# Kernel optimization log

Hardware: AMD Instinct MI355X
Metric: run time of the kernel (lower is better)

Reference implementation:

```python
import jax, jax.numpy as jnp
import numpy as np

BETA_THRESH = 0.1   # threshold fraction in forward
BETA_IPOT = 0.5     # IPOT entropic beta
ITERATION = 30


def setup_inputs() -> dict:
    key = jax.random.key(0)
    k1, k2 = jax.random.split(key)
    bs, n, m, d = 64, 512, 512, 768
    return {
        "local_features_1": jax.random.normal(k1, (bs, n, d), dtype=jnp.float32),
        "local_features_2": jax.random.normal(k2, (bs, m, d), dtype=jnp.float32),
    }


def _wasserstein_loss(x, y):
    # x: (bs, n, d), y: (bs, m, d)
    # cost_matrix_batch_torch normalizes over the feature dim (dim=1 of bs*d*n layout)
    xn = x / (jnp.linalg.norm(x, axis=2, keepdims=True) + 1e-12)
    yn = y / (jnp.linalg.norm(y, axis=2, keepdims=True) + 1e-12)
    # cost_matrix returns (1 - cos).transpose(2,1); forward transposes back -> (bs, n, m)
    cos_distance = 1.0 - jnp.einsum("bnd,bmd->bnm", xn, yn)
    # global min/max threshold + relu
    min_score = cos_distance.min()
    max_score = cos_distance.max()
    threshold = min_score + BETA_THRESH * (max_score - min_score)
    C = jax.nn.relu(cos_distance - threshold)  # (bs, n, m)
    bs, n, m = C.shape
    A = jnp.exp(-C / BETA_IPOT)
    T0 = jnp.ones((bs, n, m), dtype=C.dtype)
    sigma0 = jnp.full((bs, m, 1), 1.0 / m, dtype=C.dtype)

    def step(carry, _):
        T, sigma = carry
        Q = A * T                                      # (bs, n, m)
        delta = 1.0 / (n * jnp.matmul(Q, sigma))       # (bs, n, 1)
        a = jnp.matmul(jnp.swapaxes(Q, 1, 2), delta)   # (bs, m, 1)
        sigma = 1.0 / (m * a)                          # (bs, m, 1)
        T = delta * Q * jnp.swapaxes(sigma, 1, 2)      # (bs, n, m)
        return (T, sigma), None

    (T, _), _ = jax.lax.scan(step, (T0, sigma0), None, length=ITERATION)
    # batch_trace(C^T @ T) == sum_ij C_ij * T_ij per batch element
    distance = jnp.einsum("bnm,bnm->b", C, T)
    # IPOT_distance returns -distance; loss is its mean
    return (-distance).mean()


def reference(local_features_1, local_features_2):
    return _wasserstein_loss(local_features_1, local_features_2)
```

## Files before the change

kernel.cpp:

```cpp
#include <hip/hip_runtime.h>
#include <hip/hip_fp16.h>

#define NN 512
#define DD 768

typedef _Float16 half8 __attribute__((ext_vector_type(8)));
typedef _Float16 half4 __attribute__((ext_vector_type(4)));
typedef _Float16 half2v __attribute__((ext_vector_type(2)));
typedef float f32x4 __attribute__((ext_vector_type(4)));

__device__ __forceinline__ int f2ord(float f) {
  int i = __float_as_int(f);
  return i < 0 ? (i ^ 0x7fffffff) : i;
}
__device__ __forceinline__ float ord2f(int i) {
  return __int_as_float(i < 0 ? (i ^ 0x7fffffff) : i);
}

__device__ __forceinline__ void glds16(const void* g, void* l) {
  __builtin_amdgcn_global_load_lds((const __attribute__((address_space(1))) void*)g,
                                   (__attribute__((address_space(3))) void*)l, 16, 0, 0);
}

__global__ __launch_bounds__(256) void k_norm(const float* __restrict__ f1,
                                              const float* __restrict__ f2,
                                              __half* __restrict__ xn,
                                              __half* __restrict__ yn,
                                              int* __restrict__ meta,
                                              int* __restrict__ cnt) {
  if (blockIdx.x == 0) {
    int t = threadIdx.x;
    if (t == 0) { meta[0] = 0x7fffffff; meta[1] = 0x80000000; cnt[1024] = 0; }
    if (t < 64) cnt[t * 16] = 0;
  }
  int row = blockIdx.x * 4 + (threadIdx.x >> 6);
  int lane = threadIdx.x & 63;
  int r = row & 32767;
  const float* src = (row < 32768 ? f1 : f2) + (size_t)r * DD;
  __half* dst = (row < 32768 ? xn : yn) + (size_t)r * DD;
  f32x4 v0 = *(const f32x4*)(src + lane * 4);
  f32x4 v1 = *(const f32x4*)(src + lane * 4 + 256);
  f32x4 v2 = *(const f32x4*)(src + lane * 4 + 512);
  float s = v0[0]*v0[0] + v0[1]*v0[1] + v0[2]*v0[2] + v0[3]*v0[3]
          + v1[0]*v1[0] + v1[1]*v1[1] + v1[2]*v1[2] + v1[3]*v1[3]
          + v2[0]*v2[0] + v2[1]*v2[1] + v2[2]*v2[2] + v2[3]*v2[3];
  #pragma unroll
  for (int m = 1; m < 64; m <<= 1) s += __shfl_xor(s, m, 64);
  float f = 1.0f / (sqrtf(s) + 1e-12f);
  union U { __half2 h2[2]; uint2 u; };
  U u0, u1, u2;
  u0.h2[0] = __floats2half2_rn(v0[0]*f, v0[1]*f); u0.h2[1] = __floats2half2_rn(v0[2]*f, v0[3]*f);
  u1.h2[0] = __floats2half2_rn(v1[0]*f, v1[1]*f); u1.h2[1] = __floats2half2_rn(v1[2]*f, v1[3]*f);
  u2.h2[0] = __floats2half2_rn(v2[0]*f, v2[1]*f); u2.h2[1] = __floats2half2_rn(v2[2]*f, v2[3]*f);
  *(uint2*)(dst + lane * 4)       = u0.u;
  *(uint2*)(dst + lane * 4 + 256) = u1.u;
  *(uint2*)(dst + lane * 4 + 512) = u2.u;
}

#define FOR16(X) X(0) X(1) X(2) X(3) X(4) X(5) X(6) X(7) X(8) X(9) X(10) X(11) X(12) X(13) X(14) X(15)

#define AGLD(p) __hip_atomic_load((p), __ATOMIC_RELAXED, __HIP_MEMORY_SCOPE_AGENT)
#define AGST(p, v) __hip_atomic_store((p), (v), __ATOMIC_RELAXED, __HIP_MEMORY_SCOPE_AGENT)

struct IpotLds {
  float xs[128];
  float ys[NN];
  _Float16 zs[NN];
  _Float16 csh[8][520];
  float wred[8];
};
union MainLds {
  _Float16 Bs[2][16384];
  _Float16 At[4][8192];
  float mm[16];
  int mmi[16];
  IpotLds ip;
};

__global__ __launch_bounds__(512, 2) void k_main(const __half* __restrict__ xn,
                                                 const __half* __restrict__ yn,
                                                 int* __restrict__ meta,
                                                 int* __restrict__ cnt,
                                                 int* __restrict__ gmm,
                                                 unsigned* __restrict__ gpart,
                                                 float* __restrict__ gdist) {
  __shared__ __align__(16) MainLds u;
  const int blk = blockIdx.x;
  const int b = blk & 63, qq = blk >> 6;
  const int tid = threadIdx.x;
  const int sv = tid >> 6, lane = tid & 63;
  const int fr = lane & 15;
  const int g8 = (lane >> 4) * 8;
  const int r0 = sv * 16;
  const int c0 = lane * 8;
  const __half* xnb = xn + ((size_t)b * NN + qq * 128 + sv * 16) * DD;
  const __half* ynb = yn + (size_t)b * NN * DD;

  f32x4 acc[32] = {};
#define STAGE(bf, kk) { \
    const __half* ys_ = ynb + (size_t)(sv * 64 + lane) * DD + (kk); \
    glds16(ys_ +  0, (char*)u.Bs[bf] +         sv * 1024); \
    glds16(ys_ +  8, (char*)u.Bs[bf] +  8192 + sv * 1024); \
    glds16(ys_ + 16, (char*)u.Bs[bf] + 16384 + sv * 1024); \
    glds16(ys_ + 24, (char*)u.Bs[bf] + 24576 + sv * 1024); }
  int buf = 0;
  STAGE(0, 0)
  half8 afp = *(const half8*)(xnb + (size_t)fr * DD + g8);
  for (int kk = 0; kk < DD; kk += 32) {
    __syncthreads();
    if (kk + 32 < DD) STAGE(buf ^ 1, kk + 32)
    half8 afc = afp;
    if (kk + 32 < DD) afp = *(const half8*)(xnb + (size_t)fr * DD + (kk + 32) + g8);
    #pragma unroll
    for (int c = 0; c < 32; ++c) {
      half8 bf = *(const half8*)(&u.Bs[buf][(lane >> 4) * 4096 + (16 * c + fr) * 8]);
      acc[c] = __builtin_amdgcn_mfma_f32_16x16x32_f16(afc, bf, acc[c], 0, 0, 0);
    }
    buf ^= 1;
  }

  float vmin = 1e30f, vmax = -1e30f;
  #pragma unroll
  for (int c = 0; c < 32; ++c) {
    #pragma unroll
    for (int r2 = 0; r2 < 4; ++r2) {
      float val = 1.0f - acc[c][r2];
      vmin = fminf(vmin, val); vmax = fmaxf(vmax, val);
    }
  }
  #pragma unroll
  for (int m = 1; m < 64; m <<= 1) {
    vmin = fminf(vmin, __shfl_xor(vmin, m, 64));
    vmax = fmaxf(vmax, __shfl_xor(vmax, m, 64));
  }
  __syncthreads();
  if (lane == 0) { u.mm[sv] = vmin; u.mm[8 + sv] = vmax; }
  __syncthreads();
  if (tid == 0) {
    float bm = u.mm[0], bx = u.mm[8];
    #pragma unroll
    for (int g = 1; g < 8; ++g) { bm = fminf(bm, u.mm[g]); bx = fmaxf(bx, u.mm[8 + g]); }
    AGST(gmm + blk, (unsigned)f2ord(bm));
    AGST(gmm + 256 + blk, (unsigned)f2ord(bx));
  }
  __syncthreads();
  if (tid == 0) {
    int* cnt2 = cnt + 1024;
    __hip_atomic_fetch_add(cnt2, 1, __ATOMIC_RELAXED, __HIP_MEMORY_SCOPE_AGENT);
    while (__hip_atomic_load(cnt2, __ATOMIC_RELAXED, __HIP_MEMORY_SCOPE_AGENT) < 256)
      __builtin_amdgcn_s_sleep(1);
  }
  __syncthreads();
  {
    int mo = (int)AGLD(gmm + tid);
    #pragma unroll
    for (int m = 1; m < 64; m <<= 1) {
      int o = __shfl_xor(mo, m, 64);
      mo = (sv < 4) ? (mo < o ? mo : o) : (mo > o ? mo : o);
    }
    if (lane == 0) u.mmi[sv] = mo;
  }
  __syncthreads();
  int gmnord = u.mmi[0], gmxord = u.mmi[4];
  #pragma unroll
  for (int g = 1; g < 4; ++g) {
    gmnord = gmnord < u.mmi[g] ? gmnord : u.mmi[g];
    gmxord = gmxord > u.mmi[4 + g] ? gmxord : u.mmi[4 + g];
  }
  const float gmn = ord2f(gmnord);
  const float gmx = ord2f(gmxord);
  const float thr = gmn + 0.1f * (gmx - gmn);

#define DECLAM(r) half8 A##r, M##r;
  FOR16(DECLAM)

#define TWRITE { \
    _Float16* reg_ = u.At[sv & 3]; \
    const int q_ = lane >> 4; \
    _Pragma("unroll") \
    for (int c = 0; c < 32; ++c) { \
      _Pragma("unroll") \
      for (int r2 = 0; r2 < 4; ++r2) { \
        float val_ = 1.0f - acc[c][r2]; \
        float a_ = __expf(-2.0f * fmaxf(val_ - thr, 0.0f)); \
        int off_ = (((4 * q_ + r2) * 1024 + (16 * c + fr) * 2) ^ (q_ << 4)) >> 1; \
        reg_[off_] = (_Float16)a_; \
      } \
    } }

#define TREAD(r) { \
    A##r = *(const half8*)((const char*)u.At[sv & 3] + \
            (((r) * 1024 + lane * 16) ^ ((((r) >> 2) & 3) << 4))); \
    M##r = A##r; }

  __syncthreads();
  if (sv < 4) TWRITE
  __syncthreads();
  if (sv < 4) { FOR16(TREAD) }
  __syncthreads();
  if (sv >= 4) TWRITE
  __syncthreads();
  if (sv >= 4) { FOR16(TREAD) }
  __syncthreads();

  if (tid < 256) *(half2v*)(u.ip.zs + 2 * tid) = (half2v){(_Float16)1.0f, (_Float16)1.0f};
  u.ip.ys[tid] = 1.0f;
  __syncthreads();

  int* mycnt = cnt + b * 16;

  #pragma unroll 1
  for (int t = 1; t <= 30; ++t) {
    half8 zv = *(const half8*)(u.ip.zs + c0);
    float rp16[16];
#define ROWP(r) { \
      half8 p = M##r * zv; \
      half4 q = p.lo + p.hi; \
      half2v q2 = q.lo + q.hi; \
      rp16[r] = (float)q2.x + (float)q2.y; }
    FOR16(ROWP)
    float c8[8];
    #pragma unroll
    for (int i = 0; i < 8; ++i) {
      float keep = (lane & 1) ? rp16[2*i+1] : rp16[2*i];
      float send = (lane & 1) ? rp16[2*i]   : rp16[2*i+1];
      c8[i] = keep + __shfl_xor(send, 1, 64);
    }
    float c4[4];
    #pragma unroll
    for (int i = 0; i < 4; ++i) {
      float keep = (lane & 2) ? c8[2*i+1] : c8[2*i];
      float send = (lane & 2) ? c8[2*i]   : c8[2*i+1];
      c4[i] = keep + __shfl_xor(send, 2, 64);
    }
    float d2[2];
    #pragma unroll
    for (int i = 0; i < 2; ++i) {
      float keep = (lane & 4) ? c4[2*i+1] : c4[2*i];
      float send = (lane & 4) ? c4[2*i]   : c4[2*i+1];
      d2[i] = keep + __shfl_xor(send, 4, 64);
    }
    float c1;
    {
      float keep = (lane & 8) ? d2[1] : d2[0];
      float send = (lane & 8) ? d2[0] : d2[1];
      c1 = keep + __shfl_xor(send, 8, 64);
    }
    c1 += __shfl_xor(c1, 16, 64);
    c1 += __shfl_xor(c1, 32, 64);
    if (lane < 16) u.ip.xs[r0 + lane] = 1.0f / c1;
    half8 cac = (half8)(_Float16)0.0f;
#define COLP(r) { _Float16 xh = (_Float16)u.ip.xs[r0 + r]; cac += M##r * xh; }
    FOR16(COLP)
    *(half8*)(&u.ip.csh[sv][c0]) = cac;
#define UPDM(r) M##r *= A##r;
    if (t < 30) { FOR16(UPDM) }
    __syncthreads();
    unsigned* gp = gpart + ((size_t)((t & 1) * 256 + blk) * 256);
    if (tid < 256) {
      float a0 = 0.0f, a1 = 0.0f;
      #pragma unroll
      for (int g = 0; g < 8; ++g) {
        half2v pv = *(const half2v*)(&u.ip.csh[g][2 * tid]);
        a0 += (float)pv.x; a1 += (float)pv.y;
      }
      __half2 ph = __floats2half2_rn(a0, a1);
      AGST(gp + tid, *reinterpret_cast<unsigned*>(&ph));
    }
    __syncthreads();
    if (tid == 0) {
      __hip_atomic_fetch_add(mycnt, 1, __ATOMIC_RELAXED, __HIP_MEMORY_SCOPE_AGENT);
      while (__hip_atomic_load(mycnt, __ATOMIC_RELAXED, __HIP_MEMORY_SCOPE_AGENT) < 4 * t)
        __builtin_amdgcn_s_sleep(1);
    }
    __syncthreads();
    if (tid < 256) {
      float a0 = 0.0f, a1 = 0.0f;
      #pragma unroll
      for (int q2 = 0; q2 < 4; ++q2) {
        unsigned v = AGLD(gpart + ((size_t)((t & 1) * 256 + b + 64 * q2) * 256) + tid);
        __half2 h = *reinterpret_cast<__half2*>(&v);
        float2 fv = __half22float2(h);
        a0 += fv.x; a1 += fv.y;
      }
      float yo0 = u.ip.ys[2 * tid], yo1 = u.ip.ys[2 * tid + 1];
      float y0 = 1.0f / a0;
      float y1 = 1.0f / a1;
      *(half2v*)(u.ip.zs + 2 * tid) = (half2v){(_Float16)(y0 * y0 / yo0), (_Float16)(y1 * y1 / yo1)};
      u.ip.ys[2 * tid] = y0; u.ip.ys[2 * tid + 1] = y1;
    }
    __syncthreads();
  }

  float contrib = 0.0f;
#define FINP(r) { \
    float rowacc = 0.0f; \
    rowacc += -0.34657359f * __log2f((float)A##r.s0) * (float)M##r.s0 * u.ip.ys[c0 + 0]; \
    rowacc += -0.34657359f * __log2f((float)A##r.s1) * (float)M##r.s1 * u.ip.ys[c0 + 1]; \
    rowacc += -0.34657359f * __log2f((float)A##r.s2) * (float)M##r.s2 * u.ip.ys[c0 + 2]; \
    rowacc += -0.34657359f * __log2f((float)A##r.s3) * (float)M##r.s3 * u.ip.ys[c0 + 3]; \
    rowacc += -0.34657359f * __log2f((float)A##r.s4) * (float)M##r.s4 * u.ip.ys[c0 + 4]; \
    rowacc += -0.34657359f * __log2f((float)A##r.s5) * (float)M##r.s5 * u.ip.ys[c0 + 5]; \
    rowacc += -0.34657359f * __log2f((float)A##r.s6) * (float)M##r.s6 * u.ip.ys[c0 + 6]; \
    rowacc += -0.34657359f * __log2f((float)A##r.s7) * (float)M##r.s7 * u.ip.ys[c0 + 7]; \
    contrib += rowacc * u.ip.xs[r0 + r]; }
  FOR16(FINP)
  #pragma unroll
  for (int m = 1; m < 64; m <<= 1) contrib += __shfl_xor(contrib, m, 64);
  if (lane == 0) u.ip.wred[sv] = contrib;
  __syncthreads();
  if (tid == 0) {
    float s2 = 0.0f;
    #pragma unroll
    for (int g = 0; g < 8; ++g) s2 += u.ip.wred[g];
    gdist[blk] = s2;
  }
}

__global__ void k_final(const float* __restrict__ gdist, float* __restrict__ out) {
  int b = threadIdx.x & 63;
  float v = gdist[b] + gdist[b + 64] + gdist[b + 128] + gdist[b + 192];
  #pragma unroll
  for (int m = 1; m < 64; m <<= 1) v += __shfl_xor(v, m, 64);
  if (threadIdx.x == 0) out[0] = -v * (1.0f / (64.0f * 512.0f));
}

extern "C" void kernel_launch(void* const* d_in, const int* in_sizes, int n_in,
                              void* d_out, int out_size, void* d_ws, size_t ws_size,
                              hipStream_t stream) {
  const float* f1 = (const float*)d_in[0];
  const float* f2 = (const float*)d_in[1];
  char* ws = (char*)d_ws;
  __half* xn   = (__half*)(ws + 0);
  __half* yn   = (__half*)(ws + 50331648);
  unsigned* gpart = (unsigned*)(ws + 100663296);
  int*   meta  = (int*)(ws + 167772160);
  int*   cnt   = (int*)(ws + 167772160 + 256);
  int*   gmm   = (int*)(ws + 167772160 + 256 + 8192);
  float* gdist = (float*)(ws + 167772160 + 256 + 8192 + 2048);

  k_norm<<<16384, 256, 0, stream>>>(f1, f2, xn, yn, meta, cnt);
  k_main<<<256, 512, 0, stream>>>(xn, yn, meta, cnt, (int*)gmm, gpart, gdist);
  k_final<<<1, 64, 0, stream>>>(gdist, (float*)d_out);
}
```

Measured before the change: 222.5 us.

## Swizzle B-tile LDS layout and fold final reduction into main kernel

The global-to-LDS staging of the y tile is reorganised. Each wave now loads 16 rows times 4 chunks with an XOR-swizzled source offset, and the MFMA B-fragment reads use a matching swizzled slot. The goal is to cut LDS bank conflicts and keep global loads coalesced. The separate k_final launch is also removed: each block bumps an atomic counter, and block 0 spins until the counter reaches its target before doing the batch reduction. This saves a kernel launch but adds a spin-wait that depends on every block being co-resident and on the counter being reset correctly.

```diff
diff --git a/kernel.cpp b/kernel.cpp
--- a/kernel.cpp
+++ b/kernel.cpp
@@ -83,26 +83,30 @@
                                                  int* __restrict__ cnt,
                                                  int* __restrict__ gmm,
                                                  unsigned* __restrict__ gpart,
-                                                 float* __restrict__ gdist) {
+                                                 float* __restrict__ gdist,
+                                                 float* __restrict__ out) {
   __shared__ __align__(16) MainLds u;
   const int blk = blockIdx.x;
   const int b = blk & 63, qq = blk >> 6;
   const int tid = threadIdx.x;
   const int sv = tid >> 6, lane = tid & 63;
   const int fr = lane & 15;
-  const int g8 = (lane >> 4) * 8;
   const int r0 = sv * 16;
   const int c0 = lane * 8;
+  const int kg = lane >> 4;
+  const int g8 = kg * 8;
+  const int rslot = (kg ^ ((fr >> 1) & 3)) * 8;
   const __half* xnb = xn + ((size_t)b * NN + qq * 128 + sv * 16) * DD;
   const __half* ynb = yn + (size_t)b * NN * DD;
 
   f32x4 acc[32] = {};
+  const int srcq = ((lane & 3) ^ ((lane >> 3) & 3)) * 8;
 #define STAGE(bf, kk) { \
-    const __half* ys_ = ynb + (size_t)(sv * 64 + lane) * DD + (kk); \
-    glds16(ys_ +  0, (char*)u.Bs[bf] +         sv * 1024); \
-    glds16(ys_ +  8, (char*)u.Bs[bf] +  8192 + sv * 1024); \
-    glds16(ys_ + 16, (char*)u.Bs[bf] + 16384 + sv * 1024); \
-    glds16(ys_ + 24, (char*)u.Bs[bf] + 24576 + sv * 1024); }
+    _Pragma("unroll") \
+    for (int j = 0; j < 4; ++j) { \
+      const __half* ys_ = ynb + (size_t)(128 * j + sv * 16 + (lane >> 2)) * DD + (kk) + srcq; \
+      glds16(ys_, (char*)u.Bs[bf] + j * 8192 + sv * 1024); \
+    } }
   int buf = 0;
   STAGE(0, 0)
   half8 afp = *(const half8*)(xnb + (size_t)fr * DD + g8);
@@ -113,7 +117,7 @@
     if (kk + 32 < DD) afp = *(const half8*)(xnb + (size_t)fr * DD + (kk + 32) + g8);
     #pragma unroll
     for (int c = 0; c < 32; ++c) {
-      half8 bf = *(const half8*)(&u.Bs[buf][(lane >> 4) * 4096 + (16 * c + fr) * 8]);
+      half8 bf = *(const half8*)(&u.Bs[buf][(16 * c + fr) * 32 + rslot]);
       acc[c] = __builtin_amdgcn_mfma_f32_16x16x32_f16(afc, bf, acc[c], 0, 0, 0);
     }
     buf ^= 1;
@@ -313,16 +317,25 @@
     float s2 = 0.0f;
     #pragma unroll
     for (int g = 0; g < 8; ++g) s2 += u.ip.wred[g];
-    gdist[blk] = s2;
-  }
-}
-
-__global__ void k_final(const float* __restrict__ gdist, float* __restrict__ out) {
-  int b = threadIdx.x & 63;
-  float v = gdist[b] + gdist[b + 64] + gdist[b + 128] + gdist[b + 192];
-  #pragma unroll
-  for (int m = 1; m < 64; m <<= 1) v += __shfl_xor(v, m, 64);
-  if (threadIdx.x == 0) out[0] = -v * (1.0f / (64.0f * 512.0f));
+    AGST(gdist + blk, s2);
+  }
+  __syncthreads();
+  if (tid == 0)
+    __hip_atomic_fetch_add(cnt + 1024, 1, __ATOMIC_RELAXED, __HIP_MEMORY_SCOPE_AGENT);
+  if (blk == 0) {
+    if (tid == 0) {
+      while (__hip_atomic_load(cnt + 1024, __ATOMIC_RELAXED, __HIP_MEMORY_SCOPE_AGENT) < 512)
+        __builtin_amdgcn_s_sleep(1);
+    }
+    __syncthreads();
+    if (tid < 64) {
+      float v = AGLD(gdist + tid) + AGLD(gdist + tid + 64)
+              + AGLD(gdist + tid + 128) + AGLD(gdist + tid + 192);
+      #pragma unroll
+      for (int m = 1; m < 64; m <<= 1) v += __shfl_xor(v, m, 64);
+      if (tid == 0) out[0] = -v * (1.0f / (64.0f * 512.0f));
+    }
+  }
 }
 
 extern "C" void kernel_launch(void* const* d_in, const int* in_sizes, int n_in,
@@ -340,6 +353,6 @@
   float* gdist = (float*)(ws + 167772160 + 256 + 8192 + 2048);
 
   k_norm<<<16384, 256, 0, stream>>>(f1, f2, xn, yn, meta, cnt);
-  k_main<<<256, 512, 0, stream>>>(xn, yn, meta, cnt, (int*)gmm, gpart, gdist);
-  k_final<<<1, 64, 0, stream>>>(gdist, (float*)d_out);
-}
+  k_main<<<256, 512, 0, stream>>>(xn, yn, meta, cnt, (int*)gmm, gpart, gdist,
+                                  (float*)d_out);
+}
```

Result: faster. 193.0 us (-13.3%).
